# Kernel tuning notes

Hardware: AMD Instinct MI355X
Metric: run time of the kernel (lower is better)

Reference implementation:

```python
import jax, jax.numpy as jnp
import numpy as np

GRID_SIZE = 5
K = 3  # spline order
WIDTH = [512, 1024, 1024, 1024, 256]
BATCH = 4096


def make_grid(in_dim):
    # pykan-style extended uniform grid on [-1, 1]: G + 2K + 1 knots per input dim
    h = 2.0 / GRID_SIZE
    pts = jnp.arange(-K, GRID_SIZE + K + 1, dtype=jnp.float32) * h - 1.0
    return jnp.tile(pts[None, :], (in_dim, 1))


def bspline_basis(x, grid):
    # Cox-de Boor recursion. x: [B, in], grid: [in, G+2K+1] -> basis [B, in, G+K]
    xe = x[..., None]
    b = ((xe >= grid[:, :-1]) & (xe < grid[:, 1:])).astype(x.dtype)  # degree 0: [B, in, G+2K]
    for d in range(1, K + 1):
        left = (xe - grid[:, :-(d + 1)]) / (grid[:, d:-1] - grid[:, :-(d + 1)]) * b[..., :-1]
        right = (grid[:, d + 1:] - xe) / (grid[:, d + 1:] - grid[:, 1:-d]) * b[..., 1:]
        b = left + right
    return b


def kan_layer(x, grid, coef, scale_base, scale_sp):
    # out_j = sum_i scale_base[i,j]*silu(x_i) + scale_sp[i,j]*sum_g coef[i,j,g]*B_g(x_i)
    basis = bspline_basis(x, grid)                                   # [B, in, G+K]
    base = jnp.einsum('bi,io->bo', jax.nn.silu(x), scale_base)
    spline = jnp.einsum('big,iog->bo', basis, coef * scale_sp[:, :, None])
    return base + spline


def setup_inputs() -> dict:
    key = jax.random.key(0)
    n_layers = len(WIDTH) - 1
    keys = jax.random.split(key, 2 + 2 * n_layers)
    inp = {
        'inputs_y': jax.random.normal(keys[0], (BATCH, 256), dtype=jnp.float32) * 0.5,
        'inputs_u': jax.random.normal(keys[1], (BATCH, 256), dtype=jnp.float32) * 0.5,
    }
    for l, (din, dout) in enumerate(zip(WIDTH[:-1], WIDTH[1:])):
        inp[f'coef{l}'] = jax.random.normal(keys[2 + 2 * l], (din, dout, GRID_SIZE + K), dtype=jnp.float32) * (0.1 / np.sqrt(din))
        inp[f'sb{l}'] = jax.random.normal(keys[3 + 2 * l], (din, dout), dtype=jnp.float32) * (1.0 / np.sqrt(din))
        inp[f'ss{l}'] = jnp.ones((din, dout), dtype=jnp.float32)
        inp[f'grid{l}'] = make_grid(din)
    return inp


def reference(inputs_y, inputs_u,
              coef0, sb0, ss0, grid0,
              coef1, sb1, ss1, grid1,
              coef2, sb2, ss2, grid2,
              coef3, sb3, ss3, grid3):
    x = jnp.concatenate([inputs_y.astype(jnp.float32), inputs_u.astype(jnp.float32)], axis=-1)
    layers = [(grid0, coef0, sb0, ss0), (grid1, coef1, sb1, ss1),
              (grid2, coef2, sb2, ss2), (grid3, coef3, sb3, ss3)]
    for g, c, sb, ss in layers:
        x = kan_layer(x, g, c, sb, ss)
    return x
```

## Files before the change

kernel.cpp:

```cpp
#include <hip/hip_runtime.h>
#include <cstdint>
#include <cstddef>

typedef _Float16 f16;
typedef _Float16 f16x4 __attribute__((ext_vector_type(4)));
typedef _Float16 f16x8 __attribute__((ext_vector_type(8)));
typedef float f32x4 __attribute__((ext_vector_type(4)));

__device__ __forceinline__ void gl2lds16(const void* g, void* l) {
  __builtin_amdgcn_global_load_lds(
      (const __attribute__((address_space(1))) void*)(uintptr_t)g,
      (__attribute__((address_space(3))) void*)(uintptr_t)l,
      16, 0, 0);
}

__global__ __launch_bounds__(256) void kan_prep2(
    const float* __restrict__ coef, const float* __restrict__ sb,
    const float* __restrict__ ss, f16* __restrict__ Wt,
    int out, int K9)
{
  __shared__ float s_sb[32][32];
  __shared__ float s_ss[32][32];
  __shared__ f16 s_w[32][288];
  const int t  = threadIdx.x;
  const int o0 = blockIdx.x * 32, i0 = blockIdx.y * 32;

  {
    int il = t >> 3, oc = (t & 7) * 4;
    float4 vb = *(const float4*)(sb + (size_t)(i0 + il) * out + o0 + oc);
    float4 vs = *(const float4*)(ss + (size_t)(i0 + il) * out + o0 + oc);
    s_sb[il][oc + 0] = vb.x; s_sb[il][oc + 1] = vb.y;
    s_sb[il][oc + 2] = vb.z; s_sb[il][oc + 3] = vb.w;
    s_ss[il][oc + 0] = vs.x; s_ss[il][oc + 1] = vs.y;
    s_ss[il][oc + 2] = vs.z; s_ss[il][oc + 3] = vs.w;
  }
  __syncthreads();

#pragma unroll
  for (int j = 0; j < 8; ++j) {
    int f  = j * 256 + t;
    int il = f >> 6, c = f & 63;
    int ol = c >> 1, gh = (c & 1) * 4;
    float4 v = *(const float4*)(coef + ((size_t)(i0 + il) * out + (o0 + ol)) * 8 + gh);
    float ssv = s_ss[il][ol];
    f16* dst = &s_w[ol][il * 9 + 1 + gh];
    dst[0] = (f16)(v.x * ssv); dst[1] = (f16)(v.y * ssv);
    dst[2] = (f16)(v.z * ssv); dst[3] = (f16)(v.w * ssv);
  }
#pragma unroll
  for (int j = 0; j < 4; ++j) {
    int e = j * 256 + t; int il = e >> 5, ol = e & 31;
    s_w[ol][il * 9] = (f16)s_sb[il][ol];
  }
  __syncthreads();

  {
    int o = t >> 3, part = t & 7;
    f16* dst = Wt + (size_t)(o0 + o) * K9 + (size_t)i0 * 9 + part * 36;
    const f16* src = &s_w[o][part * 36];
#pragma unroll
    for (int q = 0; q < 9; ++q)
      *(f16x4*)(dst + q * 4) = *(const f16x4*)(src + q * 4);
  }
}

__global__ __launch_bounds__(256) void kan_feat(
    const float* __restrict__ X, f16* __restrict__ F,
    int shift, int K9, int iBase)
{
  int idx = blockIdx.x * 256 + threadIdx.x;
  int b  = idx >> shift;
  int ii = idx & ((1 << shift) - 1);
  float x = X[idx];

  float sig  = 1.0f / (1.0f + __expf(-x));
  float silu = x * sig;

  float t[12];
#pragma unroll
  for (int j = 0; j < 12; ++j) t[j] = (float)(j - 3) * 0.4f - 1.0f;
  float b0[11];
#pragma unroll
  for (int j = 0; j < 11; ++j)
    b0[j] = (x >= t[j] && x < t[j + 1]) ? 1.0f : 0.0f;
  float b1[10];
#pragma unroll
  for (int j = 0; j < 10; ++j)
    b1[j] = (x - t[j]) * 2.5f * b0[j] + (t[j + 2] - x) * 2.5f * b0[j + 1];
  float b2[9];
#pragma unroll
  for (int j = 0; j < 9; ++j)
    b2[j] = (x - t[j]) * 1.25f * b1[j] + (t[j + 3] - x) * 1.25f * b1[j + 1];
  float b3[8];
#pragma unroll
  for (int j = 0; j < 8; ++j)
    b3[j] = (x - t[j]) * (1.0f / 1.2f) * b2[j] +
            (t[j + 4] - x) * (1.0f / 1.2f) * b2[j + 1];

  f16* o = F + (size_t)b * K9 + (size_t)(iBase + ii) * 9;
  o[0] = (f16)silu;
#pragma unroll
  for (int g = 0; g < 8; ++g) o[1 + g] = (f16)b3[g];
}

#define BARRIER() do { asm volatile("" ::: "memory"); \
    __builtin_amdgcn_s_barrier(); asm volatile("" ::: "memory"); } while (0)
#define LGKM0() asm volatile("s_waitcnt lgkmcnt(0)" ::: "memory")
#define VMC4()  asm volatile("s_waitcnt vmcnt(4)" ::: "memory")
#define VMC0()  asm volatile("s_waitcnt vmcnt(0)" ::: "memory")

#define STG_A(h, tile) do { size_t _o = (size_t)(h) * hK + (size_t)(tile) * 64; \
    f16* _d = L + ((((tile) & 1) << 15) + ((h) << 13)); \
    gl2lds16(gA[0] + _o, _d + stO0); gl2lds16(gA[1] + _o, _d + stO1); } while (0)
#define STG_B(h, tile) do { size_t _o = (size_t)(h) * hK + (size_t)(tile) * 64; \
    f16* _d = L + ((((tile) & 1) << 15) + 16384 + ((h) << 13)); \
    gl2lds16(gB[0] + _o, _d + stO0); gl2lds16(gB[1] + _o, _d + stO1); } while (0)

#define RD_ALO(pa) do { _Pragma("unroll") for (int i = 0; i < 4; ++i) { \
    a[2*i]   = *(const f16x8*)((pa) + i * 1024 + fo0); \
    a[2*i+1] = *(const f16x8*)((pa) + i * 1024 + fo1); } } while (0)
#define RD_AHI(pa) do { _Pragma("unroll") for (int i = 0; i < 4; ++i) { \
    a[2*i]   = *(const f16x8*)((pa) + 4096 + i * 1024 + fo0); \
    a[2*i+1] = *(const f16x8*)((pa) + 4096 + i * 1024 + fo1); } } while (0)
#define RD_BLO(pb) do { _Pragma("unroll") for (int i = 0; i < 2; ++i) { \
    b[2*i]   = *(const f16x8*)((pb) + i * 1024 + fo0); \
    b[2*i+1] = *(const f16x8*)((pb) + i * 1024 + fo1); } } while (0)
#define RD_BHI(pb) do { _Pragma("unroll") for (int i = 0; i < 2; ++i) { \
    b[4+2*i] = *(const f16x8*)((pb) + (2 + i) * 1024 + fo0); \
    b[5+2*i] = *(const f16x8*)((pb) + (2 + i) * 1024 + fo1); } } while (0)

#define MFMA_Q(MH, NH) do { \
  __builtin_amdgcn_s_setprio(1); \
  _Pragma("unroll") for (int kk = 0; kk < 2; ++kk) \
  _Pragma("unroll") for (int mi = 0; mi < 4; ++mi) \
  _Pragma("unroll") for (int ni = 0; ni < 2; ++ni) \
    acc[(MH)*4+mi][(NH)*2+ni] = __builtin_amdgcn_mfma_f32_16x16x32_f16( \
        a[2*mi+kk], b[2*((NH)*2+ni)+kk], acc[(MH)*4+mi][(NH)*2+ni], 0, 0, 0); \
  __builtin_amdgcn_s_setprio(0); } while (0)

template <int SPLITK>
__global__ __launch_bounds__(512, 2) void kan_gemm8(
    const f16* __restrict__ A, const f16* __restrict__ Bt,
    float* __restrict__ C, int N, int K)
{
  __shared__ __align__(16) f16 lds[65536];
  f16* L = lds;
  const int tid  = threadIdx.x;
  const int lane = tid & 63;
  const int w    = tid >> 6;
  const int waveM = w >> 2, waveN = w & 3;
  const int l16 = lane & 15, quad = lane >> 4;
  const size_t mBase = (size_t)blockIdx.y * 256;
  const size_t nBase = (size_t)blockIdx.x * 256;
  const int kChunk = K / SPLITK;
  const int k0  = blockIdx.z * kChunk;
  const int nkt = kChunk >> 6;
  const size_t hK = 128 * (size_t)K;

  const f16* gA[2]; const f16* gB[2];
  {
    int c0 = tid,        r0 = c0 >> 3, p0 = c0 & 7;
    int c1 = 512 + tid,  r1 = c1 >> 3, p1 = c1 & 7;
    gA[0] = A  + (mBase + r0) * (size_t)K + k0 + (p0 ^ ((r0 >> 1) & 7)) * 8;
    gA[1] = A  + (mBase + r1) * (size_t)K + k0 + (p1 ^ ((r1 >> 1) & 7)) * 8;
    gB[0] = Bt + (nBase + r0) * (size_t)K + k0 + (p0 ^ ((r0 >> 1) & 7)) * 8;
    gB[1] = Bt + (nBase + r1) * (size_t)K + k0 + (p1 ^ ((r1 >> 1) & 7)) * 8;
  }
  const int stO0 = (tid & ~63) * 8;
  const int stO1 = (512 + (tid & ~63)) * 8;

  const int s3  = l16 >> 1;
  const int fo0 = l16 * 64 + ((quad ^ s3) & 7) * 8;
  const int fo1 = l16 * 64 + (((quad + 4) ^ s3) & 7) * 8;
  const int slotA = waveM * 8192;
  const int slotB = 16384 + (waveN >> 1) * 8192 + (waveN & 1) * 4096;

  f32x4 acc[8][4] = {};

  STG_A(0, 0); STG_A(1, 0); STG_B(0, 0); STG_B(1, 0);
  STG_B(0, 1); STG_B(1, 1);
  VMC4();
  BARRIER();

#pragma unroll 1
  for (int it = 0; it < (nkt >> 1); ++it) {
    const int t = it * 2;
    const bool nl = (t + 2) < nkt;
    f16x8 a[8], b[8];

    {
      const f16* pa = L + ((t & 1) << 15) + slotA;
      const f16* pb = L + ((t & 1) << 15) + slotB;
      RD_ALO(pa); RD_BLO(pb);
      STG_A(0, t + 1);
      BARRIER(); LGKM0(); MFMA_Q(0, 0); BARRIER();
      RD_BHI(pb);
      STG_A(1, t + 1);
      BARRIER(); LGKM0(); MFMA_Q(0, 1); BARRIER();
      RD_AHI(pa);
      if (nl) STG_B(0, t + 2);
      BARRIER(); LGKM0(); MFMA_Q(1, 1); BARRIER();
      if (nl) { STG_B(1, t + 2); VMC4(); } else { VMC0(); }
      BARRIER(); MFMA_Q(1, 0); BARRIER();
    }
    {
      const f16* pa = L + (((t + 1) & 1) << 15) + slotA;
      const f16* pb = L + (((t + 1) & 1) << 15) + slotB;
      RD_ALO(pa); RD_BLO(pb);
      if (nl) STG_A(0, t + 2);
      BARRIER(); LGKM0(); MFMA_Q(0, 0); BARRIER();
      RD_BHI(pb);
      if (nl) STG_A(1, t + 2);
      BARRIER(); LGKM0(); MFMA_Q(0, 1); BARRIER();
      RD_AHI(pa);
      if (nl) STG_B(0, t + 3);
      BARRIER(); LGKM0(); MFMA_Q(1, 1); BARRIER();
      if (nl) { STG_B(1, t + 3); VMC4(); } else { VMC0(); }
      BARRIER(); MFMA_Q(1, 0); BARRIER();
    }
  }

#pragma unroll
  for (int mi = 0; mi < 8; ++mi) {
    size_t row = mBase + waveM * 128 + mi * 16 + quad * 4;
#pragma unroll
    for (int ni = 0; ni < 4; ++ni) {
      size_t col = nBase + waveN * 64 + ni * 16 + l16;
#pragma unroll
      for (int r = 0; r < 4; ++r)
        unsafeAtomicAdd(C + (row + r) * N + col, acc[mi][ni][r]);
    }
  }
}

extern "C" void kernel_launch(void* const* d_in, const int* in_sizes, int n_in,
                              void* d_out, int out_size, void* d_ws, size_t ws_size,
                              hipStream_t stream)
{
  const float* y = (const float*)d_in[0];
  const float* u = (const float*)d_in[1];
  const float* coef[4]; const float* sb[4]; const float* ss[4];
  for (int l = 0; l < 4; ++l) {
    coef[l] = (const float*)d_in[2 + 4 * l];
    sb[l]   = (const float*)d_in[3 + 4 * l];
    ss[l]   = (const float*)d_in[4 + 4 * l];
  }
  char* ws = (char*)d_ws;
  f16*   Wt   = (f16*)(ws);
  f16*   F    = (f16*)(ws + 18874368);
  float* actA = (float*)(ws + 18874368 + 75497472);
  float* actB = (float*)(ws + 18874368 + 75497472 + 16777216);
  float* out  = (float*)d_out;
  const size_t actBytes = (size_t)4096 * 1024 * 4;

  kan_prep2<<<dim3(32, 16), 256, 0, stream>>>(coef[0], sb[0], ss[0], Wt, 1024, 4608);
  kan_feat<<<4096 * 256 / 256, 256, 0, stream>>>(y, F, 8, 4608, 0);
  kan_feat<<<4096 * 256 / 256, 256, 0, stream>>>(u, F, 8, 4608, 256);
  hipMemsetAsync(actA, 0, actBytes, stream);
  kan_gemm8<4><<<dim3(4, 16, 4), 512, 0, stream>>>(F, Wt, actA, 1024, 4608);

  kan_prep2<<<dim3(32, 32), 256, 0, stream>>>(coef[1], sb[1], ss[1], Wt, 1024, 9216);
  kan_feat<<<4096 * 1024 / 256, 256, 0, stream>>>(actA, F, 10, 9216, 0);
  hipMemsetAsync(actB, 0, actBytes, stream);
  kan_gemm8<4><<<dim3(4, 16, 4), 512, 0, stream>>>(F, Wt, actB, 1024, 9216);

  kan_prep2<<<dim3(32, 32), 256, 0, stream>>>(coef[2], sb[2], ss[2], Wt, 1024, 9216);
  kan_feat<<<4096 * 1024 / 256, 256, 0, stream>>>(actB, F, 10, 9216, 0);
  hipMemsetAsync(actA, 0, actBytes, stream);
  kan_gemm8<4><<<dim3(4, 16, 4), 512, 0, stream>>>(F, Wt, actA, 1024, 9216);

  kan_prep2<<<dim3(8, 32), 256, 0, stream>>>(coef[3], sb[3], ss[3], Wt, 256, 9216);
  kan_feat<<<4096 * 1024 / 256, 256, 0, stream>>>(actA, F, 10, 9216, 0);
  hipMemsetAsync(d_out, 0, (size_t)out_size * sizeof(float), stream);
  kan_gemm8<12><<<dim3(1, 16, 12), 512, 0, stream>>>(F, Wt, out, 256, 9216);
}
```

Before: 635.7 us.

## Software-pipeline LDS fragment reads across MFMA quadrants with split register sets

Restructures the GEMM main loop so LDS reads for the next quadrant (and the next K tile's first A/B fragments) are issued before the current MFMA batch, using separate aX/aY and blo/bhi register sets. The old loop waited on LDS reads right before each MFMA quadrant. The new one overlaps ds_reads with MFMA execution and cuts barriers from eight to four per tile. The extra fragment registers raise VGPR pressure under launch_bounds(512,2), which may cause spills. The reordered global-to-LDS staging also changes the hazards on the shared buffers.

```diff
diff --git a/kernel.cpp b/kernel.cpp
--- a/kernel.cpp
+++ b/kernel.cpp
@@ -116,26 +116,22 @@
     f16* _d = L + ((((tile) & 1) << 15) + 16384 + ((h) << 13)); \
     gl2lds16(gB[0] + _o, _d + stO0); gl2lds16(gB[1] + _o, _d + stO1); } while (0)
 
-#define RD_ALO(pa) do { _Pragma("unroll") for (int i = 0; i < 4; ++i) { \
-    a[2*i]   = *(const f16x8*)((pa) + i * 1024 + fo0); \
-    a[2*i+1] = *(const f16x8*)((pa) + i * 1024 + fo1); } } while (0)
-#define RD_AHI(pa) do { _Pragma("unroll") for (int i = 0; i < 4; ++i) { \
-    a[2*i]   = *(const f16x8*)((pa) + 4096 + i * 1024 + fo0); \
-    a[2*i+1] = *(const f16x8*)((pa) + 4096 + i * 1024 + fo1); } } while (0)
-#define RD_BLO(pb) do { _Pragma("unroll") for (int i = 0; i < 2; ++i) { \
-    b[2*i]   = *(const f16x8*)((pb) + i * 1024 + fo0); \
-    b[2*i+1] = *(const f16x8*)((pb) + i * 1024 + fo1); } } while (0)
-#define RD_BHI(pb) do { _Pragma("unroll") for (int i = 0; i < 2; ++i) { \
-    b[4+2*i] = *(const f16x8*)((pb) + (2 + i) * 1024 + fo0); \
-    b[5+2*i] = *(const f16x8*)((pb) + (2 + i) * 1024 + fo1); } } while (0)
-
-#define MFMA_Q(MH, NH) do { \
+#define RD_A_TO(dst, p, OFS) do { _Pragma("unroll") \
+  for (int i = 0; i < 4; ++i) { \
+    dst[2*i]   = *(const f16x8*)((p) + (OFS) + i * 1024 + fo0); \
+    dst[2*i+1] = *(const f16x8*)((p) + (OFS) + i * 1024 + fo1); } } while (0)
+#define RD_B_TO(dst, p, OFS) do { _Pragma("unroll") \
+  for (int i = 0; i < 2; ++i) { \
+    dst[2*i]   = *(const f16x8*)((p) + (OFS) + i * 1024 + fo0); \
+    dst[2*i+1] = *(const f16x8*)((p) + (OFS) + i * 1024 + fo1); } } while (0)
+
+#define MFMA_SET(AR, BR, MH, NH) do { \
   __builtin_amdgcn_s_setprio(1); \
   _Pragma("unroll") for (int kk = 0; kk < 2; ++kk) \
   _Pragma("unroll") for (int mi = 0; mi < 4; ++mi) \
   _Pragma("unroll") for (int ni = 0; ni < 2; ++ni) \
     acc[(MH)*4+mi][(NH)*2+ni] = __builtin_amdgcn_mfma_f32_16x16x32_f16( \
-        a[2*mi+kk], b[2*((NH)*2+ni)+kk], acc[(MH)*4+mi][(NH)*2+ni], 0, 0, 0); \
+        (AR)[2*mi+kk], (BR)[2*ni+kk], acc[(MH)*4+mi][(NH)*2+ni], 0, 0, 0); \
   __builtin_amdgcn_s_setprio(0); } while (0)
 
 template <int SPLITK>
@@ -176,48 +172,49 @@
   const int slotB = 16384 + (waveN >> 1) * 8192 + (waveN & 1) * 4096;
 
   f32x4 acc[8][4] = {};
+  f16x8 aX[8], aY[8], blo[4], bhi[4];
 
   STG_A(0, 0); STG_A(1, 0); STG_B(0, 0); STG_B(1, 0);
   STG_B(0, 1); STG_B(1, 1);
   VMC4();
   BARRIER();
+  {
+    const f16* pa = L + slotA;
+    const f16* pb = L + slotB;
+    RD_A_TO(aX, pa, 0);
+    RD_B_TO(blo, pb, 0);
+  }
+  STG_A(0, 1); STG_A(1, 1);
 
 #pragma unroll 1
-  for (int it = 0; it < (nkt >> 1); ++it) {
-    const int t = it * 2;
-    const bool nl = (t + 2) < nkt;
-    f16x8 a[8], b[8];
-
-    {
-      const f16* pa = L + ((t & 1) << 15) + slotA;
-      const f16* pb = L + ((t & 1) << 15) + slotB;
-      RD_ALO(pa); RD_BLO(pb);
-      STG_A(0, t + 1);
-      BARRIER(); LGKM0(); MFMA_Q(0, 0); BARRIER();
-      RD_BHI(pb);
-      STG_A(1, t + 1);
-      BARRIER(); LGKM0(); MFMA_Q(0, 1); BARRIER();
-      RD_AHI(pa);
-      if (nl) STG_B(0, t + 2);
-      BARRIER(); LGKM0(); MFMA_Q(1, 1); BARRIER();
-      if (nl) { STG_B(1, t + 2); VMC4(); } else { VMC0(); }
-      BARRIER(); MFMA_Q(1, 0); BARRIER();
-    }
-    {
-      const f16* pa = L + (((t + 1) & 1) << 15) + slotA;
-      const f16* pb = L + (((t + 1) & 1) << 15) + slotB;
-      RD_ALO(pa); RD_BLO(pb);
-      if (nl) STG_A(0, t + 2);
-      BARRIER(); LGKM0(); MFMA_Q(0, 0); BARRIER();
-      RD_BHI(pb);
-      if (nl) STG_A(1, t + 2);
-      BARRIER(); LGKM0(); MFMA_Q(0, 1); BARRIER();
-      RD_AHI(pa);
-      if (nl) STG_B(0, t + 3);
-      BARRIER(); LGKM0(); MFMA_Q(1, 1); BARRIER();
-      if (nl) { STG_B(1, t + 3); VMC4(); } else { VMC0(); }
-      BARRIER(); MFMA_Q(1, 0); BARRIER();
-    }
+  for (int t = 0; t < nkt; ++t) {
+    const f16* pa  = L + ((t & 1) << 15) + slotA;
+    const f16* pb  = L + ((t & 1) << 15) + slotB;
+    const f16* paN = L + (((t + 1) & 1) << 15) + slotA;
+    const f16* pbN = L + (((t + 1) & 1) << 15) + slotB;
+    const bool stg = (t + 2) < nkt;
+    const bool rdn = (t + 1) < nkt;
+
+    LGKM0();
+    RD_B_TO(bhi, pb, 2048);
+    MFMA_SET(aX, blo, 0, 0);
+    BARRIER();
+
+    LGKM0();
+    RD_A_TO(aY, pa, 4096);
+    MFMA_SET(aX, bhi, 0, 1);
+    BARRIER();
+
+    LGKM0();
+    if (stg) { STG_B(0, t + 2); STG_B(1, t + 2); VMC4(); } else { VMC0(); }
+    MFMA_SET(aY, bhi, 1, 1);
+    BARRIER();
+
+    if (rdn) RD_A_TO(aX, paN, 0);
+    if (stg) { STG_A(0, t + 2); STG_A(1, t + 2); }
+    MFMA_SET(aY, blo, 1, 0);
+    if (rdn) RD_B_TO(blo, pbN, 0);
+    BARRIER();
   }
 
 #pragma unroll
```

New measurement: 635.8 us. About the same (+0.0%).
